# Kernel tuning notes

Measured on AMD Instinct MI355X. Metric: run time of the kernel, lower is better.

## Reference

```python
import jax, jax.numpy as jnp
from jax import lax
import numpy as np

DIM = 512        # query feature dim (c)
V_DIM = 512      # key/value feature dim (c_v)
NUM_HEADS = 8
SR = 2           # sr_ratio
B, H, W = 4, 56, 56
N = H * W        # 3136 tokens
LN_EPS = 1e-5


def setup_inputs() -> dict:
    key = jax.random.key(0)
    ks = jax.random.split(key, 10)
    s = 0.02
    return {
        "x": jax.random.normal(ks[0], (B, N, DIM), jnp.float32),
        "v": jax.random.normal(ks[1], (B, N, V_DIM), jnp.float32),
        "h": H,
        "w": W,
        # weights stored [in, out] (transpose of torch Linear layout)
        "q_w": jax.random.normal(ks[2], (DIM, V_DIM), jnp.float32) * s,
        "kv_w": jax.random.normal(ks[3], (V_DIM, 2 * V_DIM), jnp.float32) * s,
        "sr_w": jax.random.normal(ks[4], (V_DIM, V_DIM, SR, SR), jnp.float32) * s,  # OIHW
        "sr_b": jax.random.normal(ks[5], (V_DIM,), jnp.float32) * s,
        "ln_g": jnp.ones((V_DIM,), jnp.float32),
        "ln_b": jnp.zeros((V_DIM,), jnp.float32),
        "proj_w": jax.random.normal(ks[6], (V_DIM, V_DIM), jnp.float32) * s,
        "proj_b": jax.random.normal(ks[7], (V_DIM,), jnp.float32) * s,
    }


def reference(x, v, h, w, q_w, kv_w, sr_w, sr_b, ln_g, ln_b, proj_w, proj_b):
    b, n, c = x.shape
    b_v, n_v, c_v = v.shape
    nh = NUM_HEADS
    dh = c_v // nh
    scale = (c // nh) ** -0.5  # head_dim from query dim, as in the torch code

    # q projection -> [b, nh, n, dh]
    q = (x @ q_w).reshape(b, n, nh, dh).transpose(0, 2, 1, 3)

    # SR path: conv(stride SR) + LayerNorm on KV tokens
    kv_ = v.transpose(0, 2, 1).reshape(b_v, c_v, h, w)            # NCHW
    kv_ = lax.conv_general_dilated(
        kv_, sr_w, window_strides=(SR, SR), padding="VALID",
        dimension_numbers=("NCHW", "OIHW", "NCHW"),
    ) + sr_b[None, :, None, None]
    kv_ = kv_.reshape(b_v, c_v, -1).transpose(0, 2, 1)            # [b, n_kv, c_v]
    mu = jnp.mean(kv_, axis=-1, keepdims=True)
    var = jnp.mean(jnp.square(kv_ - mu), axis=-1, keepdims=True)
    kv_ = (kv_ - mu) * lax.rsqrt(var + LN_EPS) * ln_g + ln_b

    # kv projection -> k, v each [b, nh, n_kv, dh]
    n_kv = kv_.shape[1]
    kv = (kv_ @ kv_w).reshape(b_v, n_kv, 2, nh, dh).transpose(2, 0, 3, 1, 4)
    k, vv = kv[0], kv[1]

    # attention (dropout prob 0 -> identity)
    attn = jax.nn.softmax(jnp.einsum("bhqd,bhkd->bhqk", q, k) * scale, axis=-1)
    out = jnp.einsum("bhqk,bhkd->bhqd", attn, vv)
    out = out.transpose(0, 2, 1, 3).reshape(b, n, c_v)

    return out @ proj_w + proj_b
```

## Files before the change

### kernel.cpp

```cpp
#include <hip/hip_runtime.h>

#define BATCH 4
#define HH    56
#define WW    56
#define NTOK  3136
#define NKV   784
#define CD    512
#define NH    8
#define DH    64
#define SCALE 0.125f

static const size_t OFF_Q   = 0;
static const size_t OFF_SCR = 6422528;
static const size_t OFF_KV  = 12845056;
static const size_t OFF_KVP = 14450688;
static const size_t OFF_SWT = 17661952;

__global__ void srwt_k(const float* __restrict__ w, float* __restrict__ out) {
    int idx = blockIdx.x * blockDim.x + threadIdx.x;
    int o = idx & 511;
    int rest = idx >> 9;
    int i = rest & 511;
    int p = rest >> 9;
    out[idx] = w[(((size_t)o * 512 + i) << 2) + p];
}

__global__ void im2col_k(const float* __restrict__ v, float* __restrict__ out) {
    int idx = blockIdx.x * blockDim.x + threadIdx.x;
    int i = idx & 511;
    int p = (idx >> 9) & 3;
    int t = idx >> 11;
    int b = t / NKV;
    int tt = t - b * NKV;
    int oy = tt / 28, ox = tt - (tt / 28) * 28;
    int ky = p >> 1, kx = p & 1;
    int y = oy * 2 + ky, x = ox * 2 + kx;
    out[idx] = v[((size_t)b * NTOK + y * WW + x) * CD + i];
}

__global__ __launch_bounds__(256) void gemm64(
    const float* __restrict__ A, const float* __restrict__ Bm,
    const float* __restrict__ bias, float* __restrict__ C,
    int M, int N, int K)
{
    __shared__ float As[16][68];
    __shared__ float Bs[16][68];
    const int tid = threadIdx.x;
    const int bn = blockIdx.x * 64;
    const int bm = blockIdx.y * 64;
    const int tx = tid & 15, ty = tid >> 4;
    const int la_c = tid & 15, la_r = tid >> 4;
    const int lb_c = tid & 63, lb_r = tid >> 6;
    float acc[4][4] = {};
    for (int k0 = 0; k0 < K; k0 += 16) {
        #pragma unroll
        for (int r = 0; r < 4; ++r)
            As[la_c][la_r + 16 * r] = A[(size_t)(bm + la_r + 16 * r) * K + k0 + la_c];
        #pragma unroll
        for (int r = 0; r < 4; ++r)
            Bs[lb_r + 4 * r][lb_c] = Bm[(size_t)(k0 + lb_r + 4 * r) * N + bn + lb_c];
        __syncthreads();
        #pragma unroll
        for (int kk = 0; kk < 16; ++kk) {
            float4 av = *(const float4*)&As[kk][ty * 4];
            float4 bv = *(const float4*)&Bs[kk][tx * 4];
            float a[4] = {av.x, av.y, av.z, av.w};
            float b[4] = {bv.x, bv.y, bv.z, bv.w};
            #pragma unroll
            for (int i = 0; i < 4; ++i)
                #pragma unroll
                for (int j = 0; j < 4; ++j)
                    acc[i][j] = fmaf(a[i], b[j], acc[i][j]);
        }
        __syncthreads();
    }
    #pragma unroll
    for (int i = 0; i < 4; ++i) {
        int row = bm + ty * 4 + i;
        int col = bn + tx * 4;
        float b0 = bias ? bias[col + 0] : 0.f;
        float b1 = bias ? bias[col + 1] : 0.f;
        float b2 = bias ? bias[col + 2] : 0.f;
        float b3 = bias ? bias[col + 3] : 0.f;
        float4 o = make_float4(acc[i][0] + b0, acc[i][1] + b1,
                               acc[i][2] + b2, acc[i][3] + b3);
        *(float4*)&C[(size_t)row * N + col] = o;
    }
}

__global__ __launch_bounds__(256) void ln_k(float* __restrict__ x,
    const float* __restrict__ g, const float* __restrict__ bta)
{
    int t = blockIdx.x;
    float* row = x + (size_t)t * CD;
    int tid = threadIdx.x;
    float2 xv = *(float2*)&row[tid * 2];
    float s  = xv.x + xv.y;
    float s2 = xv.x * xv.x + xv.y * xv.y;
    #pragma unroll
    for (int off = 32; off > 0; off >>= 1) {
        s  += __shfl_down(s, off);
        s2 += __shfl_down(s2, off);
    }
    __shared__ float sa[4], sb[4];
    int wid = tid >> 6, lane = tid & 63;
    if (lane == 0) { sa[wid] = s; sb[wid] = s2; }
    __syncthreads();
    if (tid == 0) {
        float S = sa[0] + sa[1] + sa[2] + sa[3];
        float S2 = sb[0] + sb[1] + sb[2] + sb[3];
        sa[0] = S; sb[0] = S2;
    }
    __syncthreads();
    float mu  = sa[0] * (1.f / 512.f);
    float var = sb[0] * (1.f / 512.f) - mu * mu;
    float inv = rsqrtf(var + 1e-5f);
    float2 gv = *(const float2*)&g[tid * 2];
    float2 bv = *(const float2*)&bta[tid * 2];
    xv.x = (xv.x - mu) * inv * gv.x + bv.x;
    xv.y = (xv.y - mu) * inv * gv.y + bv.y;
    *(float2*)&row[tid * 2] = xv;
}

#define CHUNK 56
__global__ __launch_bounds__(64) void attn_k(
    const float* __restrict__ q, const float* __restrict__ kvp,
    float* __restrict__ out)
{
    __shared__ float Ks[CHUNK][64];
    __shared__ float Vs[CHUNK][64];
    const int qb = blockIdx.x;
    const int h  = blockIdx.y;
    const int b  = blockIdx.z;
    const int tid = threadIdx.x;
    const int r = qb * 64 + tid;
    const float* qrow = q + ((size_t)(b * NTOK + r)) * CD + h * DH;
    float qr[64];
    #pragma unroll
    for (int d4 = 0; d4 < 16; ++d4) {
        float4 t = *(const float4*)&qrow[d4 * 4];
        qr[d4*4+0] = t.x; qr[d4*4+1] = t.y; qr[d4*4+2] = t.z; qr[d4*4+3] = t.w;
    }
    float acc[64];
    #pragma unroll
    for (int d = 0; d < 64; ++d) acc[d] = 0.f;
    float denom = 0.f;
    for (int s0 = 0; s0 < NKV; s0 += CHUNK) {
        if (tid < CHUNK) {
            const float* kp = kvp + ((size_t)(b * NKV + s0 + tid)) * 1024 + h * DH;
            #pragma unroll
            for (int d4 = 0; d4 < 16; ++d4) {
                *(float4*)&Ks[tid][d4 * 4] = *(const float4*)&kp[d4 * 4];
                *(float4*)&Vs[tid][d4 * 4] = *(const float4*)&kp[512 + d4 * 4];
            }
        }
        __syncthreads();
        for (int j = 0; j < CHUNK; ++j) {
            float p0 = 0.f, p1 = 0.f, p2 = 0.f, p3 = 0.f;
            #pragma unroll
            for (int d4 = 0; d4 < 16; ++d4) {
                float4 k4 = *(const float4*)&Ks[j][d4 * 4];
                p0 = fmaf(qr[d4*4+0], k4.x, p0);
                p1 = fmaf(qr[d4*4+1], k4.y, p1);
                p2 = fmaf(qr[d4*4+2], k4.z, p2);
                p3 = fmaf(qr[d4*4+3], k4.w, p3);
            }
            float sc = (p0 + p1) + (p2 + p3);
            float p = __expf(sc * SCALE);
            denom += p;
            #pragma unroll
            for (int d4 = 0; d4 < 16; ++d4) {
                float4 v4 = *(const float4*)&Vs[j][d4 * 4];
                acc[d4*4+0] = fmaf(p, v4.x, acc[d4*4+0]);
                acc[d4*4+1] = fmaf(p, v4.y, acc[d4*4+1]);
                acc[d4*4+2] = fmaf(p, v4.z, acc[d4*4+2]);
                acc[d4*4+3] = fmaf(p, v4.w, acc[d4*4+3]);
            }
        }
        __syncthreads();
    }
    float invd = 1.f / denom;
    float* op = out + ((size_t)(b * NTOK + r)) * CD + h * DH;
    #pragma unroll
    for (int d4 = 0; d4 < 16; ++d4) {
        float4 o = make_float4(acc[d4*4+0] * invd, acc[d4*4+1] * invd,
                               acc[d4*4+2] * invd, acc[d4*4+3] * invd);
        *(float4*)&op[d4 * 4] = o;
    }
}

extern "C" void kernel_launch(void* const* d_in, const int* in_sizes, int n_in,
                              void* d_out, int out_size, void* d_ws, size_t ws_size,
                              hipStream_t stream)
{
    const float* x    = (const float*)d_in[0];
    const float* v    = (const float*)d_in[1];
    const float* q_w  = (const float*)d_in[4];
    const float* kv_w = (const float*)d_in[5];
    const float* sr_w = (const float*)d_in[6];
    const float* sr_b = (const float*)d_in[7];
    const float* ln_g = (const float*)d_in[8];
    const float* ln_b = (const float*)d_in[9];
    const float* pj_w = (const float*)d_in[10];
    const float* pj_b = (const float*)d_in[11];
    float* out = (float*)d_out;
    float* ws  = (float*)d_ws;

    float* qbuf = ws + OFF_Q;
    float* scr  = ws + OFF_SCR;
    float* kvb  = ws + OFF_KV;
    float* kvp  = ws + OFF_KVP;
    float* swt  = ws + OFF_SWT;

    srwt_k<<<(2048 * 512) / 256, 256, 0, stream>>>(sr_w, swt);
    im2col_k<<<(3136 * 2048) / 256, 256, 0, stream>>>(v, scr);
    gemm64<<<dim3(8, 49), 256, 0, stream>>>(scr, swt, sr_b, kvb, 3136, 512, 2048);
    ln_k<<<3136, 256, 0, stream>>>(kvb, ln_g, ln_b);
    gemm64<<<dim3(16, 49), 256, 0, stream>>>(kvb, kv_w, nullptr, kvp, 3136, 1024, 512);
    gemm64<<<dim3(8, 196), 256, 0, stream>>>(x, q_w, nullptr, qbuf, 12544, 512, 512);
    attn_k<<<dim3(49, 8, 4), 64, 0, stream>>>(qbuf, kvp, scr);
    gemm64<<<dim3(8, 196), 256, 0, stream>>>(scr, pj_w, pj_b, out, 12544, 512, 512);
}
```

Before: 1.198 ms.

## Split attention KV range across two waves and read K/V directly from global

The attention kernel now launches two wavefronts per block. Each wave processes half of the 784 KV tokens for the same 64 queries, and the partial numerators and denominators are combined through shared memory. The LDS staging of K/V chunks and the per-chunk barriers are removed, so every lane reads K/V rows from global memory with wave-uniform addresses that rely on the cache. The intent is to double parallelism in the latency-bound attention stage, which had only 1568 single-wave blocks. The cost is redundant global and cache traffic and some extra shared memory for the reduction.

Result: slower. 2.592 ms (+116.3%).

```diff
diff --git a/kernel.cpp b/kernel.cpp
--- a/kernel.cpp
+++ b/kernel.cpp
@@ -9,6 +9,7 @@
 #define NH    8
 #define DH    64
 #define SCALE 0.125f
+#define KVHALF 392
 
 static const size_t OFF_Q   = 0;
 static const size_t OFF_SCR = 6422528;
@@ -122,18 +123,18 @@
     *(float2*)&row[tid * 2] = xv;
 }
 
-#define CHUNK 56
-__global__ __launch_bounds__(64) void attn_k(
+__global__ __launch_bounds__(128, 3) void attn2w(
     const float* __restrict__ q, const float* __restrict__ kvp,
     float* __restrict__ out)
 {
-    __shared__ float Ks[CHUNK][64];
-    __shared__ float Vs[CHUNK][64];
+    __shared__ float Pacc[64][68];
+    __shared__ float Pden[64];
     const int qb = blockIdx.x;
     const int h  = blockIdx.y;
     const int b  = blockIdx.z;
     const int tid = threadIdx.x;
-    const int r = qb * 64 + tid;
+    const int lane = tid & 63, wv = tid >> 6;
+    const int r = qb * 64 + lane;
     const float* qrow = q + ((size_t)(b * NTOK + r)) * CD + h * DH;
     float qr[64];
     #pragma unroll
@@ -145,47 +146,47 @@
     #pragma unroll
     for (int d = 0; d < 64; ++d) acc[d] = 0.f;
     float denom = 0.f;
-    for (int s0 = 0; s0 < NKV; s0 += CHUNK) {
-        if (tid < CHUNK) {
-            const float* kp = kvp + ((size_t)(b * NKV + s0 + tid)) * 1024 + h * DH;
-            #pragma unroll
-            for (int d4 = 0; d4 < 16; ++d4) {
-                *(float4*)&Ks[tid][d4 * 4] = *(const float4*)&kp[d4 * 4];
-                *(float4*)&Vs[tid][d4 * 4] = *(const float4*)&kp[512 + d4 * 4];
-            }
-        }
-        __syncthreads();
-        for (int j = 0; j < CHUNK; ++j) {
-            float p0 = 0.f, p1 = 0.f, p2 = 0.f, p3 = 0.f;
-            #pragma unroll
-            for (int d4 = 0; d4 < 16; ++d4) {
-                float4 k4 = *(const float4*)&Ks[j][d4 * 4];
-                p0 = fmaf(qr[d4*4+0], k4.x, p0);
-                p1 = fmaf(qr[d4*4+1], k4.y, p1);
-                p2 = fmaf(qr[d4*4+2], k4.z, p2);
-                p3 = fmaf(qr[d4*4+3], k4.w, p3);
-            }
-            float sc = (p0 + p1) + (p2 + p3);
-            float p = __expf(sc * SCALE);
-            denom += p;
-            #pragma unroll
-            for (int d4 = 0; d4 < 16; ++d4) {
-                float4 v4 = *(const float4*)&Vs[j][d4 * 4];
-                acc[d4*4+0] = fmaf(p, v4.x, acc[d4*4+0]);
-                acc[d4*4+1] = fmaf(p, v4.y, acc[d4*4+1]);
-                acc[d4*4+2] = fmaf(p, v4.z, acc[d4*4+2]);
-                acc[d4*4+3] = fmaf(p, v4.w, acc[d4*4+3]);
-            }
-        }
-        __syncthreads();
-    }
-    float invd = 1.f / denom;
-    float* op = out + ((size_t)(b * NTOK + r)) * CD + h * DH;
-    #pragma unroll
-    for (int d4 = 0; d4 < 16; ++d4) {
-        float4 o = make_float4(acc[d4*4+0] * invd, acc[d4*4+1] * invd,
-                               acc[d4*4+2] * invd, acc[d4*4+3] * invd);
-        *(float4*)&op[d4 * 4] = o;
+    const float* kbase = kvp + ((size_t)(b * NKV + wv * KVHALF)) * 1024 + h * DH;
+    for (int j = 0; j < KVHALF; ++j) {
+        const float* kp = kbase + (size_t)j * 1024;
+        float p0 = 0.f, p1 = 0.f, p2 = 0.f, p3 = 0.f;
+        #pragma unroll
+        for (int d4 = 0; d4 < 16; ++d4) {
+            float4 k4 = *(const float4*)&kp[d4 * 4];
+            p0 = fmaf(qr[d4*4+0], k4.x, p0);
+            p1 = fmaf(qr[d4*4+1], k4.y, p1);
+            p2 = fmaf(qr[d4*4+2], k4.z, p2);
+            p3 = fmaf(qr[d4*4+3], k4.w, p3);
+        }
+        float p = __expf(((p0 + p1) + (p2 + p3)) * SCALE);
+        denom += p;
+        #pragma unroll
+        for (int d4 = 0; d4 < 16; ++d4) {
+            float4 v4 = *(const float4*)&kp[512 + d4 * 4];
+            acc[d4*4+0] = fmaf(p, v4.x, acc[d4*4+0]);
+            acc[d4*4+1] = fmaf(p, v4.y, acc[d4*4+1]);
+            acc[d4*4+2] = fmaf(p, v4.z, acc[d4*4+2]);
+            acc[d4*4+3] = fmaf(p, v4.w, acc[d4*4+3]);
+        }
+    }
+    if (wv == 1) {
+        #pragma unroll
+        for (int d4 = 0; d4 < 16; ++d4)
+            *(float4*)&Pacc[lane][d4 * 4] =
+                make_float4(acc[d4*4+0], acc[d4*4+1], acc[d4*4+2], acc[d4*4+3]);
+        Pden[lane] = denom;
+    }
+    __syncthreads();
+    if (wv == 0) {
+        float inv = 1.f / (denom + Pden[lane]);
+        float* op = out + ((size_t)(b * NTOK + r)) * CD + h * DH;
+        #pragma unroll
+        for (int d4 = 0; d4 < 16; ++d4) {
+            float4 o2 = *(const float4*)&Pacc[lane][d4 * 4];
+            *(float4*)&op[d4 * 4] = make_float4(
+                (acc[d4*4+0] + o2.x) * inv, (acc[d4*4+1] + o2.y) * inv,
+                (acc[d4*4+2] + o2.z) * inv, (acc[d4*4+3] + o2.w) * inv);
+        }
     }
 }
 
@@ -218,6 +219,6 @@
     ln_k<<<3136, 256, 0, stream>>>(kvb, ln_g, ln_b);
     gemm64<<<dim3(16, 49), 256, 0, stream>>>(kvb, kv_w, nullptr, kvp, 3136, 1024, 512);
     gemm64<<<dim3(8, 196), 256, 0, stream>>>(x, q_w, nullptr, qbuf, 12544, 512, 512);
-    attn_k<<<dim3(49, 8, 4), 64, 0, stream>>>(qbuf, kvp, scr);
+    attn2w<<<dim3(49, 8, 4), 128, 0, stream>>>(qbuf, kvp, scr);
     gemm64<<<dim3(8, 196), 256, 0, stream>>>(scr, pj_w, pj_b, out, 12544, 512, 512);
 }
```
